# Kernel optimization log

Measured on AMD Instinct MI355X. Metric: run time of the kernel, lower is better.

Reference implementation:

```python
import jax, jax.numpy as jnp
import numpy as np

N_ATOMS = 50000
N_NBRS = 32
R_CUTOFF = 5.0
N_BASIS = 128
N_FILTERS = 128
N_GAUSS = 25
MAX_Z = 100
MEAN = 0.0
STDDEV = 20.0


def ssp(x):
    # shifted softplus: softplus(x) - log(2)
    return jax.nn.softplus(x) - jnp.log(2.0)


def setup_inputs() -> dict:
    key = jax.random.key(0)
    ks = jax.random.split(key, 18)
    dR = jax.random.uniform(ks[0], (N_ATOMS, N_NBRS), dtype=jnp.float32) * R_CUTOFF
    Z = jax.random.randint(ks[1], (N_ATOMS,), 0, MAX_Z)
    nbr_idx = jax.random.randint(ks[2], (N_ATOMS, N_NBRS), 0, N_ATOMS)

    def p(k, shape):
        fan_in = shape[0]
        return (jax.random.normal(k, shape, dtype=jnp.float32) / np.sqrt(fan_in)).astype(jnp.float32)

    return dict(
        dR=dR, Z=Z, nbr_idx=nbr_idx,
        embed_table=jax.random.normal(ks[3], (MAX_Z, N_BASIS), dtype=jnp.float32),
        fw1=p(ks[4], (N_GAUSS, N_FILTERS)), fb1=jnp.zeros((N_FILTERS,), jnp.float32),
        fw2=p(ks[5], (N_FILTERS, N_FILTERS)), fb2=jnp.zeros((N_FILTERS,), jnp.float32),
        in2f_w=p(ks[6], (N_BASIS, N_FILTERS)),
        f2out_w1=p(ks[7], (N_FILTERS, N_BASIS)), f2out_b1=jnp.zeros((N_BASIS,), jnp.float32),
        f2out_w2=p(ks[8], (N_BASIS, N_BASIS)), f2out_b2=jnp.zeros((N_BASIS,), jnp.float32),
        mlp_w1=p(ks[9], (N_BASIS, 64)), mlp_b1=jnp.zeros((64,), jnp.float32),
        mlp_w2=p(ks[10], (64, 1)), mlp_b2=jnp.zeros((1,), jnp.float32),
    )


def reference(dR, Z, nbr_idx, embed_table, fw1, fb1, fw2, fb2, in2f_w,
              f2out_w1, f2out_b1, f2out_w2, f2out_b2,
              mlp_w1, mlp_b1, mlp_w2, mlp_b2):
    # embedding lookup: [N, B]
    x = embed_table[Z]

    # gaussian smearing of distances: [N, K, G]
    offsets = jnp.linspace(0.0, R_CUTOFF, N_GAUSS, dtype=jnp.float32)
    coeff = -0.5 / (offsets[1] - offsets[0]) ** 2
    dr_exp = jnp.exp(coeff * (dR[..., None] - offsets) ** 2)

    # filter network: Dense+ssp, Dense -> [N, K, F]
    W = ssp(jnp.einsum('nkg,gf->nkf', dr_exp, fw1) + fb1)
    W = jnp.einsum('nkf,fh->nkh', W, fw2) + fb2

    # cosine cutoff
    fcut = 0.5 * (jnp.cos(dR * jnp.pi / R_CUTOFF) + 1.0) * (dR < R_CUTOFF)
    W = W * fcut[..., None]

    # cfconv: in2f (no bias), neighbor gather, elementwise filter, sum over neighbors
    y = x @ in2f_w                    # [N, F]
    y_nbrs = y[nbr_idx]               # [N, K, F] irregular gather
    mask = (nbr_idx < N_ATOMS)[..., None]
    agg = jnp.sum(jnp.where(mask, y_nbrs * W, 0.0), axis=1)  # [N, F]

    # f2out: Dense+ssp, Dense
    v = ssp(agg @ f2out_w1 + f2out_b1) @ f2out_w2 + f2out_b2

    # residual update
    x = x + v

    # atomwise MLP [128 -> 64 -> 1] with ssp between layers
    yi = ssp(x @ mlp_w1 + mlp_b1) @ mlp_w2 + mlp_b2  # [N, 1]
    yi = yi * STDDEV + MEAN

    # aggregate (sum over atom axis), per_atom=False
    return jnp.sum(yi, axis=0)  # [1]
```

## Files before the change

kernel.cpp:

```cpp
#include <hip/hip_runtime.h>
#include <math.h>

#define N_ATOMS  50000
#define N_NBRS   32
#define N_GAUSS  25
#define RCUT     5.0f
#define TT       88
#define TROWS    32
#define NTB      3
#define MAXZ     100
#define NT32     1563
#define PBLOCKS  512
#define NPAIR    (N_ATOMS * N_NBRS)
#define PKPAD    (NT32 * 1024)
#define PKB      782
#define PI_F     3.14159265358979323846f

typedef unsigned int   uint_t;
typedef unsigned short ushort_t;
typedef _Float16 f16;
typedef f16   f16x2 __attribute__((ext_vector_type(2)));
typedef f16   f16x4 __attribute__((ext_vector_type(4)));
typedef f16   f16x8 __attribute__((ext_vector_type(8)));
typedef float f32x4 __attribute__((ext_vector_type(4)));

__device__ __forceinline__ float ssp(float x) {
  return fmaxf(x, 0.0f) + __logf(fmaf(0.5f, __expf(-fabsf(x)), 0.5f));
}
__device__ __forceinline__ f16x2 bch(uint_t u) {
  return __builtin_bit_cast(f16x2, u);
}
__device__ __forceinline__ uint_t hcb(f16x2 v) {
  return __builtin_bit_cast(uint_t, v);
}
__device__ __forceinline__ int swz(int m, int e) {
  return m * 128 + ((((e >> 3) ^ m) & 15) << 3) + (e & 7);
}

__global__ void __launch_bounds__(256, 2)
prep_all_kernel(const float* __restrict__ fw1,
                const float* __restrict__ fb1,
                const float* __restrict__ fw2,
                const float* __restrict__ fb2,
                const float* __restrict__ w1,
                const float* __restrict__ w2,
                const float* __restrict__ mw1,
                const float* __restrict__ embed,
                const float* __restrict__ in2f,
                const float* __restrict__ dR,
                const int* __restrict__ nbr,
                const int* __restrict__ Z,
                const float* __restrict__ mb2,
                f16* __restrict__ tabh,
                f16* __restrict__ ytab,
                f16* __restrict__ w1ht,
                f16* __restrict__ w2ht,
                f16* __restrict__ mw1ht,
                uint_t* __restrict__ pkAll,
                float* __restrict__ out) {
  const int tid = threadIdx.x;
  const int bid = blockIdx.x;
  if (bid == 0 && tid == 0) {
    out[0] = 20.0f * (float)N_ATOMS * mb2[0];
  }

  __shared__ float sW2[128 * 128];
  __shared__ float sH[TROWS][128];

  if (bid >= NTB + 64) {
    const int base = (bid - NTB - 64) * 2048;
    #pragma unroll
    for (int t0 = 0; t0 < 8; ++t0) {
      const int idx = base + t0 * 256 + tid;
      if (idx < PKPAD) {
        uint_t pk = 0;
        if (idx < NPAIR) {
          const float r = dR[idx];
          const int  nb = nbr[idx];
          int i0 = (int)(r * (87.0f / RCUT) + 0.5f);
          i0 = min(i0, 87);
          pk = (uint_t)i0 | ((uint_t)Z[nb] << 8);
        }
        pkAll[idx] = pk;
      }
    }
    return;
  }

  if (bid < NTB) {
    const int i0 = bid * TROWS;
    #pragma unroll
    for (int t = 0; t < 16; ++t) {
      const int e = tid + t * 256;
      ((float4*)sW2)[e] = ((const float4*)fw2)[e];
    }
    {
      const int f  = tid & 127;
      const int rh = (tid >> 7) * (TROWS / 2);
      const float delta = RCUT / (float)(N_GAUSS - 1);
      const float coeff = -0.5f / (delta * delta);
      const float b1v = fb1[f];
      for (int j = 0; j < TROWS / 2; ++j) {
        const float r = (float)(i0 + rh + j) * (RCUT / 87.0f);
        float h = b1v;
        #pragma unroll
        for (int g = 0; g < N_GAUSS; ++g) {
          const float d = r - (float)g * delta;
          h = fmaf(__expf(coeff * d * d), fw1[g * 128 + f], h);
        }
        sH[rh + j][f] = ssp(h);
      }
    }
    __syncthreads();
    {
      const int c0 = (tid & 31) * 4;
      const int rg = (tid >> 5) * 4;
      f32x4 acc[4];
      const float4 bv = *(const float4*)&fb2[c0];
      #pragma unroll
      for (int j = 0; j < 4; ++j) acc[j] = (f32x4){bv.x, bv.y, bv.z, bv.w};
      for (int k = 0; k < 128; ++k) {
        const float4 wv = *(const float4*)&sW2[k * 128 + c0];
        #pragma unroll
        for (int j = 0; j < 4; ++j) {
          const float hv = sH[rg + j][k];
          acc[j][0] = fmaf(hv, wv.x, acc[j][0]);
          acc[j][1] = fmaf(hv, wv.y, acc[j][1]);
          acc[j][2] = fmaf(hv, wv.z, acc[j][2]);
          acc[j][3] = fmaf(hv, wv.w, acc[j][3]);
        }
      }
      #pragma unroll
      for (int j = 0; j < 4; ++j) {
        const int i = i0 + rg + j;
        if (i < TT) {
          const float r = (float)i * (RCUT / 87.0f);
          const float fc = (r < RCUT) ? 0.5f * (__cosf(r * PI_F / RCUT) + 1.0f) : 0.0f;
          f16x4 o;
          #pragma unroll
          for (int c = 0; c < 4; ++c) o[c] = (f16)(acc[j][c] * fc);
          *(f16x4*)&tabh[i * 128 + c0] = o;
        }
      }
    }
  } else {
    const int cc = (bid - NTB) * 2 + (tid >> 7);
    const int i  = tid & 127;
    w1ht[cc * 128 + i] = (f16)w1[i * 128 + cc];
    w2ht[cc * 128 + i] = (f16)w2[i * 128 + cc];
    if (cc < 64) mw1ht[cc * 128 + i] = (f16)mw1[i * 64 + cc];
    float* xs = &sH[0][0] + (tid >> 7) * 128;
    xs[i] = (cc < MAXZ) ? embed[cc * 128 + i] : 0.0f;
    __syncthreads();
    if (cc < MAXZ) {
      float acc = 0.0f;
      for (int j = 0; j < 128; j += 4) {
        const float4 xv = *reinterpret_cast<const float4*>(&xs[j]);
        acc = fmaf(xv.x, in2f[(j + 0) * 128 + i], acc);
        acc = fmaf(xv.y, in2f[(j + 1) * 128 + i], acc);
        acc = fmaf(xv.z, in2f[(j + 2) * 128 + i], acc);
        acc = fmaf(xv.w, in2f[(j + 3) * 128 + i], acc);
      }
      ytab[cc * 128 + i] = (f16)acc;
    }
  }
}

__global__ void __launch_bounds__(512, 2)
fused_kernel(const uint_t* __restrict__ pkAll,
             const int* __restrict__ Z,
             const float* __restrict__ embed,
             const f16* __restrict__ tabh,
             const f16* __restrict__ ytab,
             const f16* __restrict__ w1ht, const float* __restrict__ b1,
             const f16* __restrict__ w2ht, const float* __restrict__ b2,
             const f16* __restrict__ mw1ht, const float* __restrict__ mb1,
             const float* __restrict__ mw2,
             float* __restrict__ out) {
  const int tid = threadIdx.x;
  const int w   = tid >> 6;
  const int l   = tid & 63;
  const int q   = l >> 4;
  const int cq  = l & 15;
  const int bid = blockIdx.x;

  __shared__ __align__(16) f16    sW[TT * 128];
  __shared__ __align__(16) uint_t s_pk[2][1024];
  __shared__ __align__(16) f16    aggB[2][32 * 128];
  __shared__ __align__(16) f16    sB[32 * 128];
  __shared__ __align__(16) f16    sX[32 * 128];
  __shared__ int   sZb[2][32];
  __shared__ float sRed[8];

  for (int e = tid; e < TT * 16; e += 512) ((uint4*)sW)[e] = ((const uint4*)tabh)[e];

  const int g   = w >> 2;
  const int wvg = w & 3;
  const int rc  = cq;
  const int qk  = q;
  f16x8 bw1[2][4], bw2[2][4], bwm[4];
  float bb1[2], bb2[2];
  #pragma unroll
  for (int t = 0; t < 2; ++t) {
    const int c = wvg * 32 + t * 16 + rc;
    bb1[t] = b1[c];
    bb2[t] = b2[c];
    #pragma unroll
    for (int k0i = 0; k0i < 4; ++k0i) {
      bw1[t][k0i] = *(const f16x8*)&w1ht[c * 128 + k0i * 32 + qk * 8];
      bw2[t][k0i] = *(const f16x8*)&w2ht[c * 128 + k0i * 32 + qk * 8];
    }
  }
  const int c1 = wvg * 16 + rc;
  #pragma unroll
  for (int k0i = 0; k0i < 4; ++k0i)
    bwm[k0i] = *(const f16x8*)&mw1ht[c1 * 128 + k0i * 32 + qk * 8];
  const float bm = mb1[c1];
  const float cm = mw2[c1];

  const int m = w * 4 + q;
  const char* wb = (const char*)sW   + cq * 16;
  const char* yb = (const char*)ytab + cq * 16;

  const int myChunks = (NT32 - 1 - bid) / PBLOCKS + 1;
  float vsum = 0.0f;

  f16x2 acc[4];
  uint4 twA[4], ytA[4], twB[4], ytB[4];

#define STAGE(bb, cc) { \
    const uint2 v = *(const uint2*)&pkAll[(cc) * 1024 + tid * 2]; \
    *(uint2*)&s_pk[bb][tid * 2] = v; \
    if (tid < 32) sZb[bb][tid] = ((cc) * 32 + tid < N_ATOMS) ? Z[(cc) * 32 + tid] : 0; }

#define IG(BK, bb, gi) { \
    _Pragma("unroll") \
    for (int d = 0; d < 4; ++d) { \
      const uint_t pk = s_pk[bb][m * N_NBRS + (gi) * 4 + d]; \
      tw##BK[d] = *(const uint4*)(wb + ((pk & 0xFFu) << 8)); \
      yt##BK[d] = *(const uint4*)(yb + ((pk >> 8) << 8)); \
    } }

#define CG(BK) { \
    _Pragma("unroll") \
    for (int d = 0; d < 4; ++d) { \
      acc[0] += bch(tw##BK[d].x) * bch(yt##BK[d].x); \
      acc[1] += bch(tw##BK[d].y) * bch(yt##BK[d].y); \
      acc[2] += bch(tw##BK[d].z) * bch(yt##BK[d].z); \
      acc[3] += bch(tw##BK[d].w) * bch(yt##BK[d].w); \
    } }

#define AGGW(bb) { \
    uint4 o; \
    o.x = hcb(acc[0]); o.y = hcb(acc[1]); o.z = hcb(acc[2]); o.w = hcb(acc[3]); \
    const int mm = m & 15; \
    *(uint4*)&aggB[bb][(m >> 4) * 2048 + mm * 128 + (((cq ^ mm) & 15) << 3)] = o; }

#define AFRAGP(P, k0) (*(const f16x8*)&(P)[rc * 128 + (((((k0) >> 3) + qk) ^ rc) & 15) * 8])

  STAGE(0, bid)
  if (1 < myChunks) STAGE(1, bid + PBLOCKS)
  __syncthreads();
  #pragma unroll
  for (int c = 0; c < 4; ++c) acc[c] = (f16x2)0;
  IG(A, 0, 0) IG(B, 0, 1)
  CG(A) IG(A, 0, 2)
  CG(B) IG(B, 0, 3)
  CG(A) IG(A, 0, 4)
  CG(B) IG(B, 0, 5)
  CG(A) IG(A, 0, 6)
  CG(B) IG(B, 0, 7)
  CG(A)
  CG(B)
  AGGW(0)
  __syncthreads();

  for (int s = 0; s < myChunks; ++s) {
    const int b  = s & 1;
    const int cc = bid + s * PBLOCKS;
    const bool hn = (s + 1 < myChunks);
    const int nb_ = b ^ 1;

    if (hn) {
      #pragma unroll
      for (int c = 0; c < 4; ++c) acc[c] = (f16x2)0;
    }

    if (hn) { IG(A, nb_, 0) IG(B, nb_, 1) }
    {
      const f16* aggp = &aggB[b][g * 2048];
      f32x4 dacc[2];
      #pragma unroll
      for (int t = 0; t < 2; ++t) dacc[t] = (f32x4){bb1[t], bb1[t], bb1[t], bb1[t]};
      #pragma unroll
      for (int k0i = 0; k0i < 4; ++k0i) {
        const f16x8 af = AFRAGP(aggp, k0i * 32);
        #pragma unroll
        for (int t = 0; t < 2; ++t)
          dacc[t] = __builtin_amdgcn_mfma_f32_16x16x32_f16(af, bw1[t][k0i], dacc[t], 0, 0, 0);
      }
      f16* hB = &sB[g * 2048];
      #pragma unroll
      for (int t = 0; t < 2; ++t) {
        const int c = wvg * 32 + t * 16 + rc;
        #pragma unroll
        for (int r = 0; r < 4; ++r) hB[swz(qk * 4 + r, c)] = (f16)ssp(dacc[t][r]);
      }
    }
    if (hn) { CG(A) IG(A, nb_, 2) CG(B) CG(A) }
    __syncthreads();

    if (hn) { IG(A, nb_, 3) IG(B, nb_, 4) }
    {
      const f16* hB = &sB[g * 2048];
      f16* hX = &sX[g * 2048];
      f32x4 dacc[2];
      #pragma unroll
      for (int t = 0; t < 2; ++t) dacc[t] = (f32x4){bb2[t], bb2[t], bb2[t], bb2[t]};
      #pragma unroll
      for (int k0i = 0; k0i < 4; ++k0i) {
        const f16x8 af = AFRAGP(hB, k0i * 32);
        #pragma unroll
        for (int t = 0; t < 2; ++t)
          dacc[t] = __builtin_amdgcn_mfma_f32_16x16x32_f16(af, bw2[t][k0i], dacc[t], 0, 0, 0);
      }
      #pragma unroll
      for (int t = 0; t < 2; ++t) {
        const int c = wvg * 32 + t * 16 + rc;
        #pragma unroll
        for (int r = 0; r < 4; ++r) {
          const int mm = qk * 4 + r;
          const float x = embed[(size_t)sZb[b][g * 16 + mm] * 128 + c] + dacc[t][r];
          hX[swz(mm, c)] = (f16)x;
        }
      }
    }
    if (hn) { CG(A) IG(A, nb_, 5) CG(B) CG(A) }
    __syncthreads();

    if (hn) { IG(A, nb_, 6) IG(B, nb_, 7) }
    if (s + 2 < myChunks) STAGE(b, bid + (s + 2) * PBLOCKS)
    {
      const f16* hX = &sX[g * 2048];
      f32x4 a2 = (f32x4){bm, bm, bm, bm};
      #pragma unroll
      for (int k0i = 0; k0i < 4; ++k0i)
        a2 = __builtin_amdgcn_mfma_f32_16x16x32_f16(AFRAGP(hX, k0i * 32), bwm[k0i], a2, 0, 0, 0);
      #pragma unroll
      for (int r = 0; r < 4; ++r) {
        const int atom = cc * 32 + g * 16 + qk * 4 + r;
        if (atom < N_ATOMS) vsum = fmaf(ssp(a2[r]), cm, vsum);
      }
    }
    if (hn) { CG(A) CG(B) AGGW(nb_) }
    __syncthreads();
  }
#undef STAGE
#undef IG
#undef CG
#undef AGGW
#undef AFRAGP

  #pragma unroll
  for (int o = 1; o < 64; o <<= 1) vsum += __shfl_xor(vsum, o, 64);
  if (l == 0) sRed[w] = vsum;
  __syncthreads();
  if (tid == 0) {
    float sF = 0.0f;
    #pragma unroll
    for (int i = 0; i < 8; ++i) sF += sRed[i];
    atomicAdd(out, 20.0f * sF);
  }
}

extern "C" void kernel_launch(void* const* d_in, const int* in_sizes, int n_in,
                              void* d_out, int out_size, void* d_ws, size_t ws_size,
                              hipStream_t stream) {
  const float* dR    = (const float*)d_in[0];
  const int*   Z     = (const int*)  d_in[1];
  const int*   nbr   = (const int*)  d_in[2];
  const float* embed = (const float*)d_in[3];
  const float* fw1   = (const float*)d_in[4];
  const float* fb1   = (const float*)d_in[5];
  const float* fw2   = (const float*)d_in[6];
  const float* fb2   = (const float*)d_in[7];
  const float* in2f  = (const float*)d_in[8];
  const float* w1    = (const float*)d_in[9];
  const float* b1    = (const float*)d_in[10];
  const float* w2    = (const float*)d_in[11];
  const float* b2    = (const float*)d_in[12];
  const float* mw1   = (const float*)d_in[13];
  const float* mb1   = (const float*)d_in[14];
  const float* mw2   = (const float*)d_in[15];
  const float* mb2   = (const float*)d_in[16];
  float* out = (float*)d_out;

  char* ws = (char*)d_ws;
  f16*    tabh    = (f16*)ws;
  f16*    ytab    = (f16*)(ws + (size_t)64 * 1024);
  f16*    w1ht    = (f16*)(ws + (size_t)128 * 1024);
  f16*    w2ht    = (f16*)(ws + (size_t)192 * 1024);
  f16*    mw1ht   = (f16*)(ws + (size_t)256 * 1024);
  uint_t* pkAll   = (uint_t*)(ws + (size_t)1024 * 1024);

  prep_all_kernel<<<NTB + 64 + PKB, 256, 0, stream>>>(fw1, fb1, fw2, fb2,
      w1, w2, mw1, embed, in2f, dR, nbr, Z, mb2,
      tabh, ytab, w1ht, w2ht, mw1ht, pkAll, out);
  fused_kernel<<<PBLOCKS, 512, 0, stream>>>(pkAll, Z, embed,
      tabh, ytab, w1ht, b1, w2ht, b2, mw1ht, mb1, mw2, out);
}
```

Measured before the change: 58.85 us.

## Shrink fused blocks to 256 threads processing 16-atom chunks across 1024 blocks

Halves the block size of the fused kernel so each block of 4 waves handles a 16-atom chunk instead of two 16-atom groups, and doubles the grid to 1024 blocks over 3125 chunks. Because 50000 divides evenly by 16, padding of the packed pair array and the per-atom bounds checks are removed. The intent is better load balance, shorter per-chunk critical path and more resident blocks per CU. In exchange each block still loads the full filter table into shared memory and holds all weight fragments in registers, so per-atom setup cost roughly doubles relative to work.

```diff
diff --git a/kernel.cpp b/kernel.cpp
--- a/kernel.cpp
+++ b/kernel.cpp
@@ -9,10 +9,9 @@
 #define TROWS    32
 #define NTB      3
 #define MAXZ     100
-#define NT32     1563
-#define PBLOCKS  512
+#define NCH      3125
+#define PBLOCKS  1024
 #define NPAIR    (N_ATOMS * N_NBRS)
-#define PKPAD    (NT32 * 1024)
 #define PKB      782
 #define PI_F     3.14159265358979323846f
 
@@ -72,16 +71,12 @@
     #pragma unroll
     for (int t0 = 0; t0 < 8; ++t0) {
       const int idx = base + t0 * 256 + tid;
-      if (idx < PKPAD) {
-        uint_t pk = 0;
-        if (idx < NPAIR) {
-          const float r = dR[idx];
-          const int  nb = nbr[idx];
-          int i0 = (int)(r * (87.0f / RCUT) + 0.5f);
-          i0 = min(i0, 87);
-          pk = (uint_t)i0 | ((uint_t)Z[nb] << 8);
-        }
-        pkAll[idx] = pk;
+      if (idx < NPAIR) {
+        const float r = dR[idx];
+        const int  nb = nbr[idx];
+        int i0 = (int)(r * (87.0f / RCUT) + 0.5f);
+        i0 = min(i0, 87);
+        pkAll[idx] = (uint_t)i0 | ((uint_t)Z[nb] << 8);
       }
     }
     return;
@@ -166,7 +161,7 @@
   }
 }
 
-__global__ void __launch_bounds__(512, 2)
+__global__ void __launch_bounds__(256, 2)
 fused_kernel(const uint_t* __restrict__ pkAll,
              const int* __restrict__ Z,
              const float* __restrict__ embed,
@@ -185,24 +180,22 @@
   const int bid = blockIdx.x;
 
   __shared__ __align__(16) f16    sW[TT * 128];
-  __shared__ __align__(16) uint_t s_pk[2][1024];
-  __shared__ __align__(16) f16    aggB[2][32 * 128];
-  __shared__ __align__(16) f16    sB[32 * 128];
-  __shared__ __align__(16) f16    sX[32 * 128];
-  __shared__ int   sZb[2][32];
-  __shared__ float sRed[8];
-
-  for (int e = tid; e < TT * 16; e += 512) ((uint4*)sW)[e] = ((const uint4*)tabh)[e];
-
-  const int g   = w >> 2;
-  const int wvg = w & 3;
+  __shared__ __align__(16) uint_t s_pk[2][512];
+  __shared__ __align__(16) f16    aggB[2][16 * 128];
+  __shared__ __align__(16) f16    sB[16 * 128];
+  __shared__ __align__(16) f16    sX[16 * 128];
+  __shared__ int   sZb[2][16];
+  __shared__ float sRed[4];
+
+  for (int e = tid; e < TT * 16; e += 256) ((uint4*)sW)[e] = ((const uint4*)tabh)[e];
+
   const int rc  = cq;
   const int qk  = q;
   f16x8 bw1[2][4], bw2[2][4], bwm[4];
   float bb1[2], bb2[2];
   #pragma unroll
   for (int t = 0; t < 2; ++t) {
-    const int c = wvg * 32 + t * 16 + rc;
+    const int c = w * 32 + t * 16 + rc;
     bb1[t] = b1[c];
     bb2[t] = b2[c];
     #pragma unroll
@@ -211,7 +204,7 @@
       bw2[t][k0i] = *(const f16x8*)&w2ht[c * 128 + k0i * 32 + qk * 8];
     }
   }
-  const int c1 = wvg * 16 + rc;
+  const int c1 = w * 16 + rc;
   #pragma unroll
   for (int k0i = 0; k0i < 4; ++k0i)
     bwm[k0i] = *(const f16x8*)&mw1ht[c1 * 128 + k0i * 32 + qk * 8];
@@ -222,16 +215,16 @@
   const char* wb = (const char*)sW   + cq * 16;
   const char* yb = (const char*)ytab + cq * 16;
 
-  const int myChunks = (NT32 - 1 - bid) / PBLOCKS + 1;
+  const int myChunks = (NCH - 1 - bid) / PBLOCKS + 1;
   float vsum = 0.0f;
 
   f16x2 acc[4];
   uint4 twA[4], ytA[4], twB[4], ytB[4];
 
 #define STAGE(bb, cc) { \
-    const uint2 v = *(const uint2*)&pkAll[(cc) * 1024 + tid * 2]; \
+    const uint2 v = *(const uint2*)&pkAll[(cc) * 512 + tid * 2]; \
     *(uint2*)&s_pk[bb][tid * 2] = v; \
-    if (tid < 32) sZb[bb][tid] = ((cc) * 32 + tid < N_ATOMS) ? Z[(cc) * 32 + tid] : 0; }
+    if (tid < 16) sZb[bb][tid] = Z[(cc) * 16 + tid]; }
 
 #define IG(BK, bb, gi) { \
     _Pragma("unroll") \
@@ -253,8 +246,7 @@
 #define AGGW(bb) { \
     uint4 o; \
     o.x = hcb(acc[0]); o.y = hcb(acc[1]); o.z = hcb(acc[2]); o.w = hcb(acc[3]); \
-    const int mm = m & 15; \
-    *(uint4*)&aggB[bb][(m >> 4) * 2048 + mm * 128 + (((cq ^ mm) & 15) << 3)] = o; }
+    *(uint4*)&aggB[bb][m * 128 + (((cq ^ m) & 15) << 3)] = o; }
 
 #define AFRAGP(P, k0) (*(const f16x8*)&(P)[rc * 128 + (((((k0) >> 3) + qk) ^ rc) & 15) * 8])
 
@@ -288,7 +280,7 @@
 
     if (hn) { IG(A, nb_, 0) IG(B, nb_, 1) }
     {
-      const f16* aggp = &aggB[b][g * 2048];
+      const f16* aggp = &aggB[b][0];
       f32x4 dacc[2];
       #pragma unroll
       for (int t = 0; t < 2; ++t) dacc[t] = (f32x4){bb1[t], bb1[t], bb1[t], bb1[t]};
@@ -299,12 +291,11 @@
         for (int t = 0; t < 2; ++t)
           dacc[t] = __builtin_amdgcn_mfma_f32_16x16x32_f16(af, bw1[t][k0i], dacc[t], 0, 0, 0);
       }
-      f16* hB = &sB[g * 2048];
       #pragma unroll
       for (int t = 0; t < 2; ++t) {
-        const int c = wvg * 32 + t * 16 + rc;
-        #pragma unroll
-        for (int r = 0; r < 4; ++r) hB[swz(qk * 4 + r, c)] = (f16)ssp(dacc[t][r]);
+        const int c = w * 32 + t * 16 + rc;
+        #pragma unroll
+        for (int r = 0; r < 4; ++r) sB[swz(qk * 4 + r, c)] = (f16)ssp(dacc[t][r]);
       }
     }
     if (hn) { CG(A) IG(A, nb_, 2) CG(B) CG(A) }
@@ -312,26 +303,24 @@
 
     if (hn) { IG(A, nb_, 3) IG(B, nb_, 4) }
     {
-      const f16* hB = &sB[g * 2048];
-      f16* hX = &sX[g * 2048];
       f32x4 dacc[2];
       #pragma unroll
       for (int t = 0; t < 2; ++t) dacc[t] = (f32x4){bb2[t], bb2[t], bb2[t], bb2[t]};
       #pragma unroll
       for (int k0i = 0; k0i < 4; ++k0i) {
-        const f16x8 af = AFRAGP(hB, k0i * 32);
+        const f16x8 af = AFRAGP(sB, k0i * 32);
         #pragma unroll
         for (int t = 0; t < 2; ++t)
           dacc[t] = __builtin_amdgcn_mfma_f32_16x16x32_f16(af, bw2[t][k0i], dacc[t], 0, 0, 0);
       }
       #pragma unroll
       for (int t = 0; t < 2; ++t) {
-        const int c = wvg * 32 + t * 16 + rc;
+        const int c = w * 32 + t * 16 + rc;
         #pragma unroll
         for (int r = 0; r < 4; ++r) {
           const int mm = qk * 4 + r;
-          const float x = embed[(size_t)sZb[b][g * 16 + mm] * 128 + c] + dacc[t][r];
-          hX[swz(mm, c)] = (f16)x;
+          const float x = embed[(size_t)sZb[b][mm] * 128 + c] + dacc[t][r];
+          sX[swz(mm, c)] = (f16)x;
         }
       }
     }
@@ -341,16 +330,12 @@
     if (hn) { IG(A, nb_, 6) IG(B, nb_, 7) }
     if (s + 2 < myChunks) STAGE(b, bid + (s + 2) * PBLOCKS)
     {
-      const f16* hX = &sX[g * 2048];
       f32x4 a2 = (f32x4){bm, bm, bm, bm};
       #pragma unroll
       for (int k0i = 0; k0i < 4; ++k0i)
-        a2 = __builtin_amdgcn_mfma_f32_16x16x32_f16(AFRAGP(hX, k0i * 32), bwm[k0i], a2, 0, 0, 0);
-      #pragma unroll
-      for (int r = 0; r < 4; ++r) {
-        const int atom = cc * 32 + g * 16 + qk * 4 + r;
-        if (atom < N_ATOMS) vsum = fmaf(ssp(a2[r]), cm, vsum);
-      }
+        a2 = __builtin_amdgcn_mfma_f32_16x16x32_f16(AFRAGP(sX, k0i * 32), bwm[k0i], a2, 0, 0, 0);
+      #pragma unroll
+      for (int r = 0; r < 4; ++r) vsum = fmaf(ssp(a2[r]), cm, vsum);
     }
     if (hn) { CG(A) CG(B) AGGW(nb_) }
     __syncthreads();
@@ -366,10 +351,7 @@
   if (l == 0) sRed[w] = vsum;
   __syncthreads();
   if (tid == 0) {
-    float sF = 0.0f;
-    #pragma unroll
-    for (int i = 0; i < 8; ++i) sF += sRed[i];
-    atomicAdd(out, 20.0f * sF);
+    atomicAdd(out, 20.0f * (sRed[0] + sRed[1] + sRed[2] + sRed[3]));
   }
 }
 
@@ -406,6 +388,6 @@
   prep_all_kernel<<<NTB + 64 + PKB, 256, 0, stream>>>(fw1, fb1, fw2, fb2,
       w1, w2, mw1, embed, in2f, dR, nbr, Z, mb2,
       tabh, ytab, w1ht, w2ht, mw1ht, pkAll, out);
-  fused_kernel<<<PBLOCKS, 512, 0, stream>>>(pkAll, Z, embed,
+  fused_kernel<<<PBLOCKS, 256, 0, stream>>>(pkAll, Z, embed,
       tabh, ytab, w1ht, b1, w2ht, b2, mw1ht, mb1, mw2, out);
 }
```

Result: faster. 57.02 us (-3.1%).
